# Performance work log

Hardware: AMD Instinct MI355X
Metric: run time of the kernel (lower is better)

## Reference

```python
import jax, jax.numpy as jnp
import numpy as np

N, M, D, S = 4, 256, 32, 32


def setup_inputs() -> dict:
    key = jax.random.key(0)
    k1, k2 = jax.random.split(key)
    inputs = jax.random.normal(k1, (N, M, M, D), dtype=jnp.float32)
    mask = jnp.ones((N, M, 1), dtype=bool)
    coeffs = jax.random.normal(k2, (D, S, 15), dtype=jnp.float32) * np.sqrt(2.0) / (D + S)
    diag_bias = jnp.zeros((1, S, 1, 1), dtype=jnp.float32)
    all_bias = jnp.zeros((1, S, 1, 1), dtype=jnp.float32)
    return {"inputs": inputs, "mask": mask, "coeffs": coeffs,
            "diag_bias": diag_bias, "all_bias": all_bias}


def _contractions_2_to_2(x):
    # x: [N, D, m, m]; returns list of 15 [N, D, m, m] basis tensors ('inf' normalization)
    n, d, m, _ = x.shape
    diag = jnp.diagonal(x, axis1=2, axis2=3)            # [N, D, m]
    sum_diag = jnp.sum(diag, axis=2, keepdims=True)      # [N, D, 1]
    rows = jnp.sum(x, axis=3)                            # [N, D, m]
    cols = jnp.sum(x, axis=2)                            # [N, D, m]
    tot = jnp.sum(rows, axis=2)                          # [N, D]
    eye = jnp.eye(m, dtype=x.dtype)

    def diag_embed(v):  # v: [N, D, m] -> [N, D, m, m]
        return v[..., :, None] * eye

    full = x.shape
    op1 = diag_embed(diag)
    op2 = diag_embed(jnp.broadcast_to(sum_diag, diag.shape)) / m
    op3 = diag_embed(rows) / m
    op4 = diag_embed(cols) / m
    op5 = diag_embed(jnp.broadcast_to(tot[..., None], diag.shape)) / (m ** 2)
    op6 = jnp.broadcast_to(cols[..., :, None], full) / m
    op7 = jnp.broadcast_to(rows[..., :, None], full) / m
    op8 = jnp.broadcast_to(cols[..., None, :], full) / m
    op9 = jnp.broadcast_to(rows[..., None, :], full) / m
    op10 = x
    op11 = jnp.swapaxes(x, 2, 3)
    op12 = jnp.broadcast_to(diag[..., :, None], full)
    op13 = jnp.broadcast_to(diag[..., None, :], full)
    op14 = jnp.broadcast_to(sum_diag[..., None], full) / m
    op15 = jnp.broadcast_to(tot[..., None, None], full) / (m ** 2)
    return [op1, op2, op3, op4, op5, op6, op7, op8, op9, op10,
            op11, op12, op13, op14, op15]


def reference(inputs, mask, coeffs, diag_bias, all_bias):
    # inputs: [N, m, m, D] -> [N, D, m, m]
    x = jnp.transpose(inputs, (0, 3, 1, 2))
    m = x.shape[3]
    ops = _contractions_2_to_2(x)
    # einsum('dsb,ndbij->nsij') expressed as accumulation over the 15 bases
    # (avoids materializing the [N, D, 15, m, m] stack)
    out = jnp.zeros((x.shape[0], coeffs.shape[1], m, m), dtype=x.dtype)
    for b, op in enumerate(ops):
        out = out + jnp.einsum('ds,ndij->nsij', coeffs[:, :, b], op)
    eye = jnp.eye(m, dtype=x.dtype)[None, None]
    out = out + all_bias + eye * diag_bias
    return jnp.transpose(out, (0, 2, 3, 1))  # [N, m, m, S]
```

## Files before the change

### kernel.cpp

```cpp
#include <hip/hip_runtime.h>


#define NN 4
#define MM 256
#define DD 32
#define SS 32

#define WS_ROWS   0
#define WS_DIAG   32768
#define WS_COLSP  65536
#define WS_RW     196608
#define WS_CW     229376
#define WS_DW     262144
#define WS_SD     294912
#define WS_TOT    295040
#define WS_CPACK  295168

__global__ __launch_bounds__(256) void k_reduce(const float* __restrict__ in,
                                                const float* __restrict__ coeffs,
                                                float* __restrict__ ws) {
    int blk = blockIdx.x;
    int t = threadIdx.x;
    if (blk < 128) {
        int n = blk >> 5;
        int rem = blk & 31;
        int jb = rem >> 2, ih = rem & 3;
        int i0 = ih * 64, j0 = jb * 32;
        int jl = t >> 3, d4 = t & 7;
        const float4* base = (const float4*)in;
        size_t idx0 = ((size_t)(n * MM + i0) * MM + (j0 + jl)) * 8 + d4;
        float4 a = {0.f, 0.f, 0.f, 0.f};
        #pragma unroll 8
        for (int i = 0; i < 64; ++i) {
            float4 v = base[idx0 + (size_t)i * MM * 8];
            a.x += v.x; a.y += v.y; a.z += v.z; a.w += v.w;
        }
        ((float4*)(ws + WS_COLSP))[(size_t)ih * 8192 + (n * MM + j0 + jl) * 8 + d4] = a;
    } else if (blk < 128 + NN * MM) {
        int nm = blk - 128;
        int n = nm >> 8;
        int ii = nm & 255;
        int d4 = t & 7, jg = t >> 3;
        const float4* base = (const float4*)(in + (size_t)nm * MM * DD);
        float4 a = {0.f, 0.f, 0.f, 0.f};
        #pragma unroll
        for (int k = 0; k < 8; ++k) {
            float4 v = base[(jg * 8 + k) * 8 + d4];
            a.x += v.x; a.y += v.y; a.z += v.z; a.w += v.w;
        }
        __shared__ float4 red[256];
        red[t] = a;
        __syncthreads();
        if (t < 8) {
            float4 s = {0.f, 0.f, 0.f, 0.f};
            #pragma unroll 8
            for (int g = 0; g < 32; ++g) {
                float4 v = red[g * 8 + t];
                s.x += v.x; s.y += v.y; s.z += v.z; s.w += v.w;
            }
            ((float4*)(ws + WS_ROWS))[nm * 8 + t] = s;
            float4 dv = ((const float4*)in)[((size_t)nm * MM + ii) * 8 + t];
            ((float4*)(ws + WS_DIAG))[nm * 8 + t] = dv;
            atomicAdd(ws + WS_TOT + n * DD + t * 4 + 0, s.x);
            atomicAdd(ws + WS_TOT + n * DD + t * 4 + 1, s.y);
            atomicAdd(ws + WS_TOT + n * DD + t * 4 + 2, s.z);
            atomicAdd(ws + WS_TOT + n * DD + t * 4 + 3, s.w);
            atomicAdd(ws + WS_SD + n * DD + t * 4 + 0, dv.x);
            atomicAdd(ws + WS_SD + n * DD + t * 4 + 1, dv.y);
            atomicAdd(ws + WS_SD + n * DD + t * 4 + 2, dv.z);
            atomicAdd(ws + WS_SD + n * DD + t * 4 + 3, dv.w);
        }
    } else {
        for (int idx = t; idx < 15 * DD * SS; idx += 256) {
            int plane = idx >> 10;
            int ds = idx & 1023;
            ws[WS_CPACK + plane * (DD * SS) + ds] = coeffs[ds * 15 + plane];
        }
    }
}

__global__ __launch_bounds__(256) void k_aux(const float* __restrict__ diag_bias,
                                             const float* __restrict__ all_bias,
                                             float* __restrict__ ws) {
    int idx = blockIdx.x * blockDim.x + threadIdx.x;
    int s = idx & 31;
    int nm = idx >> 5;
    int n = nm >> 8;
    const float inv_m = 1.0f / MM;
    const float inv_m2 = inv_m * inv_m;
    float u = 0.f, v = 0.f, dgacc = 0.f, w = 0.f;
    for (int d = 0; d < DD; ++d) {
        const float* cp = ws + WS_CPACK + d * SS + s;
        float r = ws[WS_ROWS + nm * DD + d];
        float cl = ws[WS_COLSP + 0 * 32768 + nm * DD + d]
                 + ws[WS_COLSP + 1 * 32768 + nm * DD + d]
                 + ws[WS_COLSP + 2 * 32768 + nm * DD + d]
                 + ws[WS_COLSP + 3 * 32768 + nm * DD + d];
        float dv = ws[WS_DIAG + nm * DD + d];
        float sdv = ws[WS_SD + n * DD + d];
        float totv = ws[WS_TOT + n * DD + d];
        u += cp[5 * 1024] * cl * inv_m + cp[6 * 1024] * r * inv_m + cp[11 * 1024] * dv;
        v += cp[7 * 1024] * cl * inv_m + cp[8 * 1024] * r * inv_m + cp[12 * 1024] * dv;
        dgacc += cp[0] * dv + cp[1 * 1024] * sdv * inv_m + cp[2 * 1024] * r * inv_m
               + cp[3 * 1024] * cl * inv_m + cp[4 * 1024] * totv * inv_m2;
        w += cp[13 * 1024] * sdv * inv_m + cp[14 * 1024] * totv * inv_m2;
    }
    ws[WS_RW + idx] = u + w + all_bias[s];
    ws[WS_CW + idx] = v;
    ws[WS_DW + idx] = dgacc + diag_bias[s];
}

__global__ __launch_bounds__(256) void k_main(const float* __restrict__ in,
                                              const float* __restrict__ ws,
                                              float* __restrict__ out) {
    int b = blockIdx.x;
    int tjb = b & 15;
    int tib = (b >> 4) & 15;
    int n = b >> 8;
    int tj = threadIdx.x & 15, ti = threadIdx.x >> 4;
    int i = tib * 16 + ti, j = tjb * 16 + tj;

    const float4* rw = (const float4*)(ws + WS_RW + (n * MM + i) * SS);
    const float4* cw = (const float4*)(ws + WS_CW + (n * MM + j) * SS);
    float4 rv[8], cv[8];
    #pragma unroll
    for (int q = 0; q < 8; ++q) rv[q] = rw[q];
    #pragma unroll
    for (int q = 0; q < 8; ++q) cv[q] = cw[q];
    __builtin_amdgcn_sched_barrier(0);

    float acc[SS];
    #pragma unroll
    for (int q = 0; q < 8; ++q) {
        acc[q * 4 + 0] = rv[q].x + cv[q].x;
        acc[q * 4 + 1] = rv[q].y + cv[q].y;
        acc[q * 4 + 2] = rv[q].z + cv[q].z;
        acc[q * 4 + 3] = rv[q].w + cv[q].w;
    }
    if (i == j) {
        const float4* dw = (const float4*)(ws + WS_DW + (n * MM + i) * SS);
        #pragma unroll
        for (int q = 0; q < 8; ++q) {
            float4 dq = dw[q];
            acc[q * 4 + 0] += dq.x;
            acc[q * 4 + 1] += dq.y;
            acc[q * 4 + 2] += dq.z;
            acc[q * 4 + 3] += dq.w;
        }
    }

    const float4* A = (const float4*)(in + (((size_t)(n * MM + i)) * MM + j) * DD);
    const float4* B = (const float4*)(in + (((size_t)(n * MM + j)) * MM + i) * DD);
    float4 av[8], bv[8];
    #pragma unroll
    for (int q = 0; q < 8; ++q) av[q] = A[q];
    #pragma unroll
    for (int q = 0; q < 8; ++q) bv[q] = B[q];
    __builtin_amdgcn_sched_barrier(0);

    const float* c10 = ws + WS_CPACK + 9 * (DD * SS);
    const float* c11 = ws + WS_CPACK + 10 * (DD * SS);
    #pragma unroll
    for (int dq = 0; dq < 8; ++dq) {
        const float* ca = c10 + dq * 4 * SS;
        const float* cb = c11 + dq * 4 * SS;
        #pragma unroll
        for (int r = 0; r < 4; ++r) {
            float a = (r == 0) ? av[dq].x : (r == 1) ? av[dq].y : (r == 2) ? av[dq].z : av[dq].w;
            float bb = (r == 0) ? bv[dq].x : (r == 1) ? bv[dq].y : (r == 2) ? bv[dq].z : bv[dq].w;
            #pragma unroll
            for (int s = 0; s < SS; ++s) {
                acc[s] = fmaf(a, ca[r * SS + s], acc[s]);
                acc[s] = fmaf(bb, cb[r * SS + s], acc[s]);
            }
        }
    }

    float4* o = (float4*)(out + (((size_t)(n * MM + i)) * MM + j) * SS);
    #pragma unroll
    for (int q = 0; q < 8; ++q)
        o[q] = make_float4(acc[q * 4 + 0], acc[q * 4 + 1], acc[q * 4 + 2], acc[q * 4 + 3]);
}

extern "C" void kernel_launch(void* const* d_in, const int* in_sizes, int n_in,
                              void* d_out, int out_size, void* d_ws, size_t ws_size,
                              hipStream_t stream) {
    const float* in = (const float*)d_in[0];
    const float* coeffs = (const float*)d_in[2];
    const float* diag_bias = (const float*)d_in[3];
    const float* all_bias = (const float*)d_in[4];
    float* out = (float*)d_out;
    float* ws = (float*)d_ws;

    hipMemsetAsync((char*)d_ws + (size_t)WS_SD * 4, 0, 256 * sizeof(float), stream);
    k_reduce<<<128 + NN * MM + 1, 256, 0, stream>>>(in, coeffs, ws);
    k_aux<<<(NN * MM * SS) / 256, 256, 0, stream>>>(diag_bias, all_bias, ws);
    k_main<<<NN * 16 * 16, 256, 0, stream>>>(in, ws, out);
}
```

Baseline: 164.0 us.

## Restructure main kernel to one row per block with LDS-staged coalesced loads/stores

The main kernel now assigns one output row (n,i) per block, with each thread handling one j. It stages the contiguous A row, the strided transposed B column, and the output tile through padded shared memory so global loads and stores are coalesced float4 accesses. The column-weight buffer is stored transposed so each thread reads it coalesced. The reduction kernel is split into separate rows and cols kernels, with column sums accumulated via atomics into a zeroed buffer. This adds extra launches, syncs and shared-memory traffic, and the B gather still reads strided 128-byte chunks.

Measured after the change: 160.1 us. 2.3% less time.

```diff
diff --git a/kernel.cpp b/kernel.cpp
--- a/kernel.cpp
+++ b/kernel.cpp
@@ -6,70 +6,83 @@
 #define DD 32
 #define SS 32
 
-#define WS_ROWS   0
-#define WS_DIAG   32768
-#define WS_COLSP  65536
-#define WS_RW     196608
-#define WS_CW     229376
-#define WS_DW     262144
-#define WS_SD     294912
-#define WS_TOT    295040
-#define WS_CPACK  295168
-
-__global__ __launch_bounds__(256) void k_reduce(const float* __restrict__ in,
-                                                const float* __restrict__ coeffs,
-                                                float* __restrict__ ws) {
-    int blk = blockIdx.x;
+#define WS_COLS   0
+#define WS_SD     32768
+#define WS_TOT    32896
+#define WS_ROWS   33024
+#define WS_DIAG   65792
+#define WS_RW     98560
+#define WS_CWT    131328
+#define WS_DW     164096
+#define WS_CPACK  196864
+
+__global__ __launch_bounds__(256) void k_rows(const float* __restrict__ in,
+                                              float* __restrict__ ws) {
+    int nm = blockIdx.x;
+    int n = nm >> 8;
+    int ii = nm & 255;
     int t = threadIdx.x;
-    if (blk < 128) {
-        int n = blk >> 5;
-        int rem = blk & 31;
-        int jb = rem >> 2, ih = rem & 3;
-        int i0 = ih * 64, j0 = jb * 32;
-        int jl = t >> 3, d4 = t & 7;
-        const float4* base = (const float4*)in;
-        size_t idx0 = ((size_t)(n * MM + i0) * MM + (j0 + jl)) * 8 + d4;
-        float4 a = {0.f, 0.f, 0.f, 0.f};
+    const float4* base = (const float4*)(in + (size_t)nm * MM * DD);
+    float4 a = {0.f, 0.f, 0.f, 0.f};
+    #pragma unroll
+    for (int k = 0; k < 8; ++k) {
+        float4 v = base[t + k * 256];
+        a.x += v.x; a.y += v.y; a.z += v.z; a.w += v.w;
+    }
+    __shared__ float4 red[256];
+    red[t] = a;
+    __syncthreads();
+    if (t < 8) {
+        float4 s = {0.f, 0.f, 0.f, 0.f};
         #pragma unroll 8
-        for (int i = 0; i < 64; ++i) {
-            float4 v = base[idx0 + (size_t)i * MM * 8];
-            a.x += v.x; a.y += v.y; a.z += v.z; a.w += v.w;
-        }
-        ((float4*)(ws + WS_COLSP))[(size_t)ih * 8192 + (n * MM + j0 + jl) * 8 + d4] = a;
-    } else if (blk < 128 + NN * MM) {
-        int nm = blk - 128;
-        int n = nm >> 8;
-        int ii = nm & 255;
-        int d4 = t & 7, jg = t >> 3;
-        const float4* base = (const float4*)(in + (size_t)nm * MM * DD);
-        float4 a = {0.f, 0.f, 0.f, 0.f};
-        #pragma unroll
-        for (int k = 0; k < 8; ++k) {
-            float4 v = base[(jg * 8 + k) * 8 + d4];
-            a.x += v.x; a.y += v.y; a.z += v.z; a.w += v.w;
-        }
-        __shared__ float4 red[256];
-        red[t] = a;
-        __syncthreads();
-        if (t < 8) {
-            float4 s = {0.f, 0.f, 0.f, 0.f};
-            #pragma unroll 8
-            for (int g = 0; g < 32; ++g) {
-                float4 v = red[g * 8 + t];
-                s.x += v.x; s.y += v.y; s.z += v.z; s.w += v.w;
-            }
-            ((float4*)(ws + WS_ROWS))[nm * 8 + t] = s;
-            float4 dv = ((const float4*)in)[((size_t)nm * MM + ii) * 8 + t];
-            ((float4*)(ws + WS_DIAG))[nm * 8 + t] = dv;
-            atomicAdd(ws + WS_TOT + n * DD + t * 4 + 0, s.x);
-            atomicAdd(ws + WS_TOT + n * DD + t * 4 + 1, s.y);
-            atomicAdd(ws + WS_TOT + n * DD + t * 4 + 2, s.z);
-            atomicAdd(ws + WS_TOT + n * DD + t * 4 + 3, s.w);
-            atomicAdd(ws + WS_SD + n * DD + t * 4 + 0, dv.x);
-            atomicAdd(ws + WS_SD + n * DD + t * 4 + 1, dv.y);
-            atomicAdd(ws + WS_SD + n * DD + t * 4 + 2, dv.z);
-            atomicAdd(ws + WS_SD + n * DD + t * 4 + 3, dv.w);
-        }
+        for (int g = 0; g < 32; ++g) {
+            float4 v = red[g * 8 + t];
+            s.x += v.x; s.y += v.y; s.z += v.z; s.w += v.w;
+        }
+        ((float4*)(ws + WS_ROWS))[nm * 8 + t] = s;
+        float4 dv = ((const float4*)in)[((size_t)nm * MM + ii) * 8 + t];
+        ((float4*)(ws + WS_DIAG))[nm * 8 + t] = dv;
+        atomicAdd(ws + WS_TOT + n * DD + t * 4 + 0, s.x);
+        atomicAdd(ws + WS_TOT + n * DD + t * 4 + 1, s.y);
+        atomicAdd(ws + WS_TOT + n * DD + t * 4 + 2, s.z);
+        atomicAdd(ws + WS_TOT + n * DD + t * 4 + 3, s.w);
+        atomicAdd(ws + WS_SD + n * DD + t * 4 + 0, dv.x);
+        atomicAdd(ws + WS_SD + n * DD + t * 4 + 1, dv.y);
+        atomicAdd(ws + WS_SD + n * DD + t * 4 + 2, dv.z);
+        atomicAdd(ws + WS_SD + n * DD + t * 4 + 3, dv.w);
+    }
+}
+
+__global__ __launch_bounds__(256) void k_cols(const float* __restrict__ in,
+                                              const float* __restrict__ coeffs,
+                                              float* __restrict__ ws) {
+    int b = blockIdx.x;
+    int t = threadIdx.x;
+    if (b < 256) {
+        int n = b >> 6, jb = (b >> 3) & 7, ic = b & 7;
+        int i0 = ic * 32, j0 = jb * 32;
+        const float4* base = (const float4*)in
+            + ((size_t)(n * MM + i0) * MM + j0) * 8 + t;
+        float4 a0 = {0,0,0,0}, a1 = {0,0,0,0}, a2 = {0,0,0,0}, a3 = {0,0,0,0};
+        #pragma unroll 4
+        for (int i = 0; i < 32; i += 4) {
+            float4 v0 = base[(size_t)(i + 0) * MM * 8];
+            float4 v1 = base[(size_t)(i + 1) * MM * 8];
+            float4 v2 = base[(size_t)(i + 2) * MM * 8];
+            float4 v3 = base[(size_t)(i + 3) * MM * 8];
+            a0.x += v0.x; a0.y += v0.y; a0.z += v0.z; a0.w += v0.w;
+            a1.x += v1.x; a1.y += v1.y; a1.z += v1.z; a1.w += v1.w;
+            a2.x += v2.x; a2.y += v2.y; a2.z += v2.z; a2.w += v2.w;
+            a3.x += v3.x; a3.y += v3.y; a3.z += v3.z; a3.w += v3.w;
+        }
+        float4 a = {a0.x + a1.x + a2.x + a3.x, a0.y + a1.y + a2.y + a3.y,
+                    a0.z + a1.z + a2.z + a3.z, a0.w + a1.w + a2.w + a3.w};
+        int j = j0 + (t >> 3), d = (t & 7) * 4;
+        float* dst = ws + WS_COLS + (n * MM + j) * DD + d;
+        atomicAdd(dst + 0, a.x);
+        atomicAdd(dst + 1, a.y);
+        atomicAdd(dst + 2, a.z);
+        atomicAdd(dst + 3, a.w);
     } else {
         for (int idx = t; idx < 15 * DD * SS; idx += 256) {
             int plane = idx >> 10;
@@ -86,16 +99,14 @@
     int s = idx & 31;
     int nm = idx >> 5;
     int n = nm >> 8;
+    int m = nm & 255;
     const float inv_m = 1.0f / MM;
     const float inv_m2 = inv_m * inv_m;
     float u = 0.f, v = 0.f, dgacc = 0.f, w = 0.f;
     for (int d = 0; d < DD; ++d) {
         const float* cp = ws + WS_CPACK + d * SS + s;
         float r = ws[WS_ROWS + nm * DD + d];
-        float cl = ws[WS_COLSP + 0 * 32768 + nm * DD + d]
-                 + ws[WS_COLSP + 1 * 32768 + nm * DD + d]
-                 + ws[WS_COLSP + 2 * 32768 + nm * DD + d]
-                 + ws[WS_COLSP + 3 * 32768 + nm * DD + d];
+        float cl = ws[WS_COLS + nm * DD + d];
         float dv = ws[WS_DIAG + nm * DD + d];
         float sdv = ws[WS_SD + n * DD + d];
         float totv = ws[WS_TOT + n * DD + d];
@@ -105,40 +116,27 @@
                + cp[3 * 1024] * cl * inv_m + cp[4 * 1024] * totv * inv_m2;
         w += cp[13 * 1024] * sdv * inv_m + cp[14 * 1024] * totv * inv_m2;
     }
-    ws[WS_RW + idx] = u + w + all_bias[s];
-    ws[WS_CW + idx] = v;
-    ws[WS_DW + idx] = dgacc + diag_bias[s];
+    ws[WS_RW + nm * SS + s] = u + w + all_bias[s];
+    ws[WS_CWT + (n * SS + s) * MM + m] = v;
+    ws[WS_DW + nm * SS + s] = dgacc + diag_bias[s];
 }
 
 __global__ __launch_bounds__(256) void k_main(const float* __restrict__ in,
                                               const float* __restrict__ ws,
                                               float* __restrict__ out) {
-    int b = blockIdx.x;
-    int tjb = b & 15;
-    int tib = (b >> 4) & 15;
-    int n = b >> 8;
-    int tj = threadIdx.x & 15, ti = threadIdx.x >> 4;
-    int i = tib * 16 + ti, j = tjb * 16 + tj;
-
-    const float4* rw = (const float4*)(ws + WS_RW + (n * MM + i) * SS);
-    const float4* cw = (const float4*)(ws + WS_CW + (n * MM + j) * SS);
-    float4 rv[8], cv[8];
-    #pragma unroll
-    for (int q = 0; q < 8; ++q) rv[q] = rw[q];
-    #pragma unroll
-    for (int q = 0; q < 8; ++q) cv[q] = cw[q];
-    __builtin_amdgcn_sched_barrier(0);
-
+    __shared__ float tile[256 * 36];
+    int nm = blockIdx.x;
+    int n = nm >> 8;
+    int i = nm & 255;
+    int t = threadIdx.x;
+
+    const float* rwp = ws + WS_RW + nm * SS;
+    const float* cwt = ws + WS_CWT + n * SS * MM + t;
     float acc[SS];
     #pragma unroll
-    for (int q = 0; q < 8; ++q) {
-        acc[q * 4 + 0] = rv[q].x + cv[q].x;
-        acc[q * 4 + 1] = rv[q].y + cv[q].y;
-        acc[q * 4 + 2] = rv[q].z + cv[q].z;
-        acc[q * 4 + 3] = rv[q].w + cv[q].w;
-    }
-    if (i == j) {
-        const float4* dw = (const float4*)(ws + WS_DW + (n * MM + i) * SS);
+    for (int s = 0; s < SS; ++s) acc[s] = rwp[s] + cwt[s * MM];
+    if (t == i) {
+        const float4* dw = (const float4*)(ws + WS_DW + nm * SS);
         #pragma unroll
         for (int q = 0; q < 8; ++q) {
             float4 dq = dw[q];
@@ -149,37 +147,74 @@
         }
     }
 
-    const float4* A = (const float4*)(in + (((size_t)(n * MM + i)) * MM + j) * DD);
-    const float4* B = (const float4*)(in + (((size_t)(n * MM + j)) * MM + i) * DD);
-    float4 av[8], bv[8];
-    #pragma unroll
-    for (int q = 0; q < 8; ++q) av[q] = A[q];
-    #pragma unroll
-    for (int q = 0; q < 8; ++q) bv[q] = B[q];
-    __builtin_amdgcn_sched_barrier(0);
+    {
+        const float4* Arow = (const float4*)(in + (size_t)nm * MM * DD);
+        #pragma unroll
+        for (int k = 0; k < 8; ++k) {
+            int idx = t + k * 256;
+            int p = idx >> 3, c = idx & 7;
+            float4 v = Arow[idx];
+            *(float4*)(tile + p * 36 + c * 4) = v;
+        }
+    }
+    __syncthreads();
 
     const float* c10 = ws + WS_CPACK + 9 * (DD * SS);
     const float* c11 = ws + WS_CPACK + 10 * (DD * SS);
+    const float* lrow = tile + t * 36;
     #pragma unroll
     for (int dq = 0; dq < 8; ++dq) {
+        float4 a4 = *(const float4*)(lrow + dq * 4);
         const float* ca = c10 + dq * 4 * SS;
+        #pragma unroll
+        for (int r = 0; r < 4; ++r) {
+            float a = (r == 0) ? a4.x : (r == 1) ? a4.y : (r == 2) ? a4.z : a4.w;
+            #pragma unroll
+            for (int s = 0; s < SS; ++s)
+                acc[s] = fmaf(a, ca[r * SS + s], acc[s]);
+        }
+    }
+    __syncthreads();
+
+    {
+        const float4* Bbase = (const float4*)in;
+        #pragma unroll
+        for (int k = 0; k < 8; ++k) {
+            int idx = t + k * 256;
+            int p = idx >> 3, c = idx & 7;
+            float4 v = Bbase[((size_t)(n * MM + p) * MM + i) * 8 + c];
+            *(float4*)(tile + p * 36 + c * 4) = v;
+        }
+    }
+    __syncthreads();
+
+    #pragma unroll
+    for (int dq = 0; dq < 8; ++dq) {
+        float4 b4 = *(const float4*)(lrow + dq * 4);
         const float* cb = c11 + dq * 4 * SS;
         #pragma unroll
         for (int r = 0; r < 4; ++r) {
-            float a = (r == 0) ? av[dq].x : (r == 1) ? av[dq].y : (r == 2) ? av[dq].z : av[dq].w;
-            float bb = (r == 0) ? bv[dq].x : (r == 1) ? bv[dq].y : (r == 2) ? bv[dq].z : bv[dq].w;
+            float bb = (r == 0) ? b4.x : (r == 1) ? b4.y : (r == 2) ? b4.z : b4.w;
             #pragma unroll
-            for (int s = 0; s < SS; ++s) {
-                acc[s] = fmaf(a, ca[r * SS + s], acc[s]);
+            for (int s = 0; s < SS; ++s)
                 acc[s] = fmaf(bb, cb[r * SS + s], acc[s]);
-            }
-        }
-    }
-
-    float4* o = (float4*)(out + (((size_t)(n * MM + i)) * MM + j) * SS);
+        }
+    }
     #pragma unroll
     for (int q = 0; q < 8; ++q)
-        o[q] = make_float4(acc[q * 4 + 0], acc[q * 4 + 1], acc[q * 4 + 2], acc[q * 4 + 3]);
+        *(float4*)(tile + t * 36 + q * 4) =
+            make_float4(acc[q * 4 + 0], acc[q * 4 + 1], acc[q * 4 + 2], acc[q * 4 + 3]);
+    __syncthreads();
+
+    {
+        float4* Orow = (float4*)(out + (size_t)nm * MM * SS);
+        #pragma unroll
+        for (int k = 0; k < 8; ++k) {
+            int idx = t + k * 256;
+            int p = idx >> 3, c = idx & 7;
+            Orow[idx] = *(const float4*)(tile + p * 36 + c * 4);
+        }
+    }
 }
 
 extern "C" void kernel_launch(void* const* d_in, const int* in_sizes, int n_in,
@@ -192,8 +227,9 @@
     float* out = (float*)d_out;
     float* ws = (float*)d_ws;
 
-    hipMemsetAsync((char*)d_ws + (size_t)WS_SD * 4, 0, 256 * sizeof(float), stream);
-    k_reduce<<<128 + NN * MM + 1, 256, 0, stream>>>(in, coeffs, ws);
+    hipMemsetAsync(d_ws, 0, (size_t)(32768 + 256) * sizeof(float), stream);
+    k_rows<<<NN * MM, 256, 0, stream>>>(in, ws);
+    k_cols<<<257, 256, 0, stream>>>(in, coeffs, ws);
     k_aux<<<(NN * MM * SS) / 256, 256, 0, stream>>>(diag_bias, all_bias, ws);
-    k_main<<<NN * 16 * 16, 256, 0, stream>>>(in, ws, out);
-}
+    k_main<<<NN * MM, 256, 0, stream>>>(in, ws, out);
+}
```
